# Performance work log

Measured on AMD Instinct MI355X. Metric: run time of the kernel, lower is better.

Reference implementation:

```python
import jax, jax.numpy as jnp
import numpy as np

B, S, D = 4, 2048, 1024
H = 16
DH = D // H          # 64
DFF = 4096
EPS = 1e-5


def _layer_norm(x, gamma, beta):
    mu = jnp.mean(x, axis=-1, keepdims=True)
    var = jnp.mean(jnp.square(x - mu), axis=-1, keepdims=True)
    return (x - mu) * jax.lax.rsqrt(var + EPS) * gamma + beta


def setup_inputs() -> dict:
    key = jax.random.key(0)
    ks = jax.random.split(key, 8)
    s_in = 1.0 / np.sqrt(D)
    s_ff = 1.0 / np.sqrt(DFF)
    return {
        "x": jax.random.normal(ks[0], (B, S, D), dtype=jnp.float32),
        # per-head qkv weights stacked: [H, D, 3*DH] (nn.Linear, bias=False)
        "Wqkv": jax.random.normal(ks[1], (H, D, 3 * DH), dtype=jnp.float32) * s_in,
        "Wproj": jax.random.normal(ks[2], (D, D), dtype=jnp.float32) * s_in,
        "bproj": jnp.zeros((D,), dtype=jnp.float32),
        "ln1_g": jnp.ones((D,), dtype=jnp.float32),
        "ln1_b": jnp.zeros((D,), dtype=jnp.float32),
        "ln2_g": jnp.ones((D,), dtype=jnp.float32),
        "ln2_b": jnp.zeros((D,), dtype=jnp.float32),
        "W1": jax.random.normal(ks[3], (D, DFF), dtype=jnp.float32) * s_in,
        "b1": jnp.zeros((DFF,), dtype=jnp.float32),
        "W2": jax.random.normal(ks[4], (DFF, D), dtype=jnp.float32) * s_ff,
        "b2": jnp.zeros((D,), dtype=jnp.float32),
    }


def reference(x, Wqkv, Wproj, bproj, ln1_g, ln1_b, ln2_g, ln2_b, W1, b1, W2, b2):
    # fused multi-head QKV projection: [B,S,D] x [H,D,3*DH] -> [B,H,S,3*DH]
    qkv = jnp.einsum('bsd,hde->bhse', x, Wqkv)
    q, k, v = jnp.split(qkv, 3, axis=-1)          # each [B,H,S,DH]
    scale = 1.0 / jnp.sqrt(jnp.asarray(DH, dtype=x.dtype))
    scores = jnp.einsum('bhsd,bhtd->bhst', q, k) * scale   # [B,H,S,S]
    causal = jnp.tril(jnp.ones((S, S), dtype=bool))
    scores = jnp.where(causal, scores, jnp.finfo(x.dtype).min)
    attn = jax.nn.softmax(scores, axis=-1)
    heads = jnp.einsum('bhst,bhtd->bhsd', attn, v)          # [B,H,S,DH]
    att_out = heads.transpose(0, 2, 1, 3).reshape(B, S, D)  # concat heads
    att_out = att_out @ Wproj + bproj
    out = _layer_norm(x + att_out, ln1_g, ln1_b)            # dropout = identity (eval)
    mlp_out = (jax.nn.gelu(out @ W1 + b1, approximate=False)) @ W2 + b2
    out = _layer_norm(out + mlp_out, ln2_g, ln2_b)
    return out
```

## Files before the change

### kernel.cpp

```cpp
#include <hip/hip_runtime.h>
#include <math.h>

#define BB 4
#define SS 2048
#define DD 1024
#define HH 16
#define DHH 64
#define DFF 4096
static constexpr float LN_EPS = 1e-5f;

typedef __bf16 bf16x8 __attribute__((ext_vector_type(8)));
typedef float f32x4 __attribute__((ext_vector_type(4)));
typedef unsigned short u16x8 __attribute__((ext_vector_type(8)));

__device__ inline unsigned short f2bf(float f) {
    union { float f; unsigned int u; } v; v.f = f;
    unsigned int u = v.u + 0x7FFFu + ((v.u >> 16) & 1u);
    return (unsigned short)(u >> 16);
}

__device__ __forceinline__ float fexp2(float x) {
    return __builtin_amdgcn_exp2f(x);
}

__device__ __forceinline__ void gl_lds16(const unsigned short* g,
                                         unsigned short* l) {
    __builtin_amdgcn_global_load_lds(
        (const __attribute__((address_space(1))) unsigned int*)g,
        (__attribute__((address_space(3))) unsigned int*)l, 16, 0, 0);
}

#define GBAR()                               \
    do {                                     \
        asm volatile("" ::: "memory");       \
        __builtin_amdgcn_s_barrier();        \
        asm volatile("" ::: "memory");       \
    } while (0)
#define VMCNT(n) asm volatile("s_waitcnt vmcnt(" #n ")" ::: "memory")

__global__ __launch_bounds__(256) void transpose_bf16_kernel(
    const float* __restrict__ in, unsigned short* __restrict__ outT,
    int R, int C) {
    __shared__ float t[64][65];
    const int r0 = blockIdx.y * 64, c0 = blockIdx.x * 64;
    const int cl = threadIdx.x & 63, rl = threadIdx.x >> 6;
#pragma unroll
    for (int rr = 0; rr < 16; ++rr)
        t[rl + rr * 4][cl] = in[(size_t)(r0 + rl + rr * 4) * C + c0 + cl];
    __syncthreads();
#pragma unroll
    for (int rr = 0; rr < 16; ++rr)
        outT[(size_t)(c0 + rl + rr * 4) * R + r0 + cl] = f2bf(t[cl][rl + rr * 4]);
}

__global__ __launch_bounds__(256) void repack_wqkv_bf16_kernel(
    const float* __restrict__ Wqkv, unsigned short* __restrict__ Wq2T) {
    __shared__ float t[64][65];
    const int h = blockIdx.z;
    const int d0 = blockIdx.y * 64, e0 = blockIdx.x * 64;
    const int cl = threadIdx.x & 63, rl = threadIdx.x >> 6;
#pragma unroll
    for (int rr = 0; rr < 16; ++rr)
        t[rl + rr * 4][cl] =
            Wqkv[((size_t)h * DD + d0 + rl + rr * 4) * 192 + e0 + cl];
    __syncthreads();
#pragma unroll
    for (int rr = 0; rr < 16; ++rr)
        Wq2T[((size_t)h * 192 + e0 + rl + rr * 4) * DD + d0 + cl] =
            f2bf(t[cl][rl + rr * 4]);
}

__global__ __launch_bounds__(256) void f2bf_kernel(
    const float* __restrict__ in, unsigned short* __restrict__ out, int n) {
    int i = blockIdx.x * 256 + threadIdx.x;
    if (i < n) out[i] = f2bf(in[i]);
}

template <int RS>
__device__ __forceinline__ void stage_half(const unsigned short* __restrict__ G,
                                           int ldK, int growbase, int kbase,
                                           unsigned short* lbase, int tid) {
#pragma unroll
    for (int s = 0; s < 2; ++s) {
        const int c16 = s * 512 + tid;
        const int r = c16 >> 3, c = c16 & 7;
        const int grow =
            growbase + ((r >> RS) << (RS + 1)) + (r & ((1 << RS) - 1));
        const int gcol = kbase + ((c ^ (r & 7)) << 3);
        gl_lds16(&G[(size_t)grow * ldK + gcol], &lbase[c16 << 3]);
    }
}

__device__ __forceinline__ void stage_64(const unsigned short* __restrict__ G,
                                         int ldK, int growbase, int kbase,
                                         unsigned short* lbase, int tid) {
    const int r = tid >> 3, c = tid & 7;
    const int grow = growbase + ((r >> 5) << 6) + (r & 31);
    const int gcol = kbase + ((c ^ (r & 7)) << 3);
    gl_lds16(&G[(size_t)grow * ldK + gcol], &lbase[tid << 3]);
}

__device__ __forceinline__ void read_afrag(const unsigned short* s, int base,
                                           int wm, int l15, int g,
                                           bf16x8 af[4][2]) {
#pragma unroll
    for (int ii = 0; ii < 4; ++ii) {
        const int lr = wm * 64 + ii * 16 + l15;
#pragma unroll
        for (int ks = 0; ks < 2; ++ks) {
            const int p = ((ks << 2) + g) ^ (lr & 7);
            af[ii][ks] = __builtin_bit_cast(
                bf16x8, *(const u16x8*)&s[base + lr * 64 + p * 8]);
        }
    }
}

__device__ __forceinline__ void read_bfrag(const unsigned short* s, int base,
                                           int wn, int l15, int g,
                                           bf16x8 bf2[2][2]) {
#pragma unroll
    for (int jj = 0; jj < 2; ++jj) {
        const int lr = wn * 32 + jj * 16 + l15;
#pragma unroll
        for (int ks = 0; ks < 2; ++ks) {
            const int p = ((ks << 2) + g) ^ (lr & 7);
            bf2[jj][ks] = __builtin_bit_cast(
                bf16x8, *(const u16x8*)&s[base + lr * 64 + p * 8]);
        }
    }
}

template <int MH, int NH>
__device__ __forceinline__ void mfma_quad(f32x4 acc[8][4],
                                          const bf16x8 af[4][2],
                                          const bf16x8 bf2[2][2]) {
    __builtin_amdgcn_s_setprio(1);
#pragma unroll
    for (int ks = 0; ks < 2; ++ks)
#pragma unroll
        for (int ii = 0; ii < 4; ++ii)
#pragma unroll
            for (int jj = 0; jj < 2; ++jj)
                acc[MH * 4 + ii][NH * 2 + jj] =
                    __builtin_amdgcn_mfma_f32_16x16x32_bf16(
                        af[ii][ks], bf2[jj][ks],
                        acc[MH * 4 + ii][NH * 2 + jj], 0, 0, 0);
    __builtin_amdgcn_s_setprio(0);
}

template <int MODE>
__global__ __launch_bounds__(512) void mfma_gemm256_kernel(
    const unsigned short* __restrict__ A, const unsigned short* __restrict__ BT,
    float* __restrict__ Cf, unsigned short* __restrict__ Cb,
    const float* __restrict__ bias, const float* __restrict__ resid,
    int M, int N, int K) {
    __shared__ __align__(16) unsigned short smem[65536];
    const int tid = threadIdx.x;
    const int lane = tid & 63, wave = tid >> 6;
    const int wm = wave >> 2, wn = wave & 3;
    const int l15 = lane & 15, g = lane >> 4;

    const int gx = gridDim.x, nwg = gx * gridDim.y;
    const int lid = blockIdx.y * gx + blockIdx.x;
    const int swz = ((nwg & 7) == 0) ? ((lid & 7) * (nwg >> 3) + (lid >> 3))
                                     : lid;
    const int row0 = (swz / gx) * 256;
    const int col0 = (swz % gx) * 256;

    const int kt = K >> 6;

    f32x4 acc[8][4] = {};

    stage_half<6>(A, K, row0, 0, smem + 0, tid);
    stage_half<6>(A, K, row0 + 64, 0, smem + 8192, tid);
    stage_half<5>(BT, K, col0, 0, smem + 32768, tid);
    stage_half<5>(BT, K, col0 + 32, 0, smem + 40960, tid);
    VMCNT(4);
    stage_half<6>(A, K, row0, 64, smem + 16384, tid);
    stage_half<6>(A, K, row0 + 64, 64, smem + 24576, tid);
    stage_half<5>(BT, K, col0, 64, smem + 49152, tid);
    VMCNT(6);
    GBAR();

    bf16x8 af[4][2], bf0[2][2], bf1[2][2];
    for (int it = 0; it < (kt >> 1); ++it) {
        const int t1k = (2 * it + 1) << 6;
        int t2 = 2 * it + 2; if (t2 > kt - 1) t2 = kt - 1;
        int t3 = 2 * it + 3; if (t3 > kt - 1) t3 = kt - 1;
        const int t2k = t2 << 6, t3k = t3 << 6;

        read_afrag(smem, 0, wm, l15, g, af);
        read_bfrag(smem, 32768, wn, l15, g, bf0);
        stage_half<5>(BT, K, col0 + 32, t1k, smem + 57344, tid);
        GBAR();
        mfma_quad<0, 0>(acc, af, bf0);
        GBAR();

        read_bfrag(smem, 40960, wn, l15, g, bf1);
        stage_half<6>(A, K, row0, t2k, smem + 0, tid);
        GBAR();
        mfma_quad<0, 1>(acc, af, bf1);
        GBAR();

        read_afrag(smem, 8192, wm, l15, g, af);
        stage_half<5>(BT, K, col0, t2k, smem + 32768, tid);
        GBAR();
        mfma_quad<1, 1>(acc, af, bf1);
        GBAR();

        stage_half<6>(A, K, row0 + 64, t2k, smem + 8192, tid);
        GBAR();
        mfma_quad<1, 0>(acc, af, bf0);
        VMCNT(6);
        GBAR();

        read_afrag(smem, 16384, wm, l15, g, af);
        read_bfrag(smem, 49152, wn, l15, g, bf0);
        stage_half<5>(BT, K, col0 + 32, t2k, smem + 40960, tid);
        GBAR();
        mfma_quad<0, 0>(acc, af, bf0);
        GBAR();

        read_bfrag(smem, 57344, wn, l15, g, bf1);
        stage_half<6>(A, K, row0, t3k, smem + 16384, tid);
        GBAR();
        mfma_quad<0, 1>(acc, af, bf1);
        GBAR();

        read_afrag(smem, 24576, wm, l15, g, af);
        stage_half<5>(BT, K, col0, t3k, smem + 49152, tid);
        GBAR();
        mfma_quad<1, 1>(acc, af, bf1);
        GBAR();

        stage_half<6>(A, K, row0 + 64, t3k, smem + 24576, tid);
        GBAR();
        mfma_quad<1, 0>(acc, af, bf0);
        VMCNT(6);
        GBAR();
    }
    VMCNT(0);
    GBAR();

    if (MODE == 2) {
        constexpr int SLAB = 264;
#pragma unroll
        for (int i2 = 0; i2 < 8; ++i2) {
            __syncthreads();
#pragma unroll
            for (int j2 = 0; j2 < 4; ++j2) {
                const int col = wn * 64 + j2 * 16 + l15;
                const float bv = bias[col0 + col];
#pragma unroll
                for (int r = 0; r < 4; ++r) {
                    float v = acc[i2][j2][r] + bv;
                    float t = fexp2(v * (2.30211849f + 0.10294198f * v * v));
                    float gel = v * t * __builtin_amdgcn_rcpf(t + 1.f);
                    smem[(wm * 16 + g * 4 + r) * SLAB + col] = f2bf(gel);
                }
            }
            __syncthreads();
            const int sr = tid >> 4;
            const int cc = (tid & 15) * 16;
            const int grow = row0 + ((sr >> 4) << 7) + i2 * 16 + (sr & 15);
            *(u16x8*)&Cb[(size_t)grow * N + col0 + cc] =
                *(const u16x8*)&smem[sr * SLAB + cc];
            *(u16x8*)&Cb[(size_t)grow * N + col0 + cc + 8] =
                *(const u16x8*)&smem[sr * SLAB + cc + 8];
        }
        return;
    }

#pragma unroll
    for (int i2 = 0; i2 < 8; ++i2) {
#pragma unroll
        for (int j2 = 0; j2 < 4; ++j2) {
            const int col = col0 + wn * 64 + j2 * 16 + l15;
            const int rowb = row0 + wm * 128 + i2 * 16 + g * 4;
            const float bv = bias[col];
#pragma unroll
            for (int r = 0; r < 4; ++r) {
                const int row = rowb + r;
                float v = acc[i2][j2][r] + bv + resid[(size_t)row * N + col];
                Cf[(size_t)row * N + col] = v;
            }
        }
    }
}

__device__ __forceinline__ void read_af128(const unsigned short* s, int base,
                                           int wm, int l15, int g,
                                           bf16x8 af[2][2]) {
#pragma unroll
    for (int ii = 0; ii < 2; ++ii) {
        const int lr = wm * 32 + ii * 16 + l15;
#pragma unroll
        for (int ks = 0; ks < 2; ++ks) {
            const int p = ((ks << 2) + g) ^ (lr & 7);
            af[ii][ks] = __builtin_bit_cast(
                bf16x8, *(const u16x8*)&s[base + lr * 64 + p * 8]);
        }
    }
}

__device__ __forceinline__ void read_bf128(const unsigned short* s, int base,
                                           int wn, int l15, int g,
                                           bf16x8 bf2[2][2]) {
#pragma unroll
    for (int jj = 0; jj < 2; ++jj) {
        const int lr = wn * 32 + jj * 16 + l15;
#pragma unroll
        for (int ks = 0; ks < 2; ++ks) {
            const int p = ((ks << 2) + g) ^ (lr & 7);
            bf2[jj][ks] = __builtin_bit_cast(
                bf16x8, *(const u16x8*)&s[base + lr * 64 + p * 8]);
        }
    }
}

template <int MH, int NH>
__device__ __forceinline__ void mfma_quad128(f32x4 acc[4][4],
                                             const bf16x8 af[2][2],
                                             const bf16x8 bf2[2][2]) {
    __builtin_amdgcn_s_setprio(1);
#pragma unroll
    for (int ks = 0; ks < 2; ++ks)
#pragma unroll
        for (int ii = 0; ii < 2; ++ii)
#pragma unroll
            for (int jj = 0; jj < 2; ++jj)
                acc[MH * 2 + ii][NH * 2 + jj] =
                    __builtin_amdgcn_mfma_f32_16x16x32_bf16(
                        af[ii][ks], bf2[jj][ks],
                        acc[MH * 2 + ii][NH * 2 + jj], 0, 0, 0);
    __builtin_amdgcn_s_setprio(0);
}

template <int MODE>
__global__ __launch_bounds__(512) void gemm_n128_kernel(
    const unsigned short* __restrict__ A, const unsigned short* __restrict__ BT,
    float* __restrict__ Cf, const float* __restrict__ bias,
    const float* __restrict__ resid, unsigned short* __restrict__ Qb,
    unsigned short* __restrict__ Kb, unsigned short* __restrict__ VTb,
    int M, int N, int K) {
    __shared__ __align__(16) unsigned short smem[49152];
    const int tid = threadIdx.x;
    const int lane = tid & 63, wave = tid >> 6;
    const int wm = wave >> 1, wn = wave & 1;
    const int l15 = lane & 15, g = lane >> 4;

    const int gx = gridDim.x, nwg = gx * gridDim.y;
    const int lid = blockIdx.y * gx + blockIdx.x;
    const int swz = ((nwg & 7) == 0) ? ((lid & 7) * (nwg >> 3) + (lid >> 3))
                                     : lid;
    const int row0 = (swz / gx) * 256;
    const int col0 = (swz % gx) * 128;

    const int kt = K >> 6;

    f32x4 acc[4][4] = {};

    stage_half<5>(A, K, row0, 0, smem + 0, tid);
    stage_half<5>(A, K, row0 + 32, 0, smem + 8192, tid);
    stage_64(BT, K, col0, 0, smem + 32768, tid);
    stage_64(BT, K, col0 + 32, 0, smem + 36864, tid);
    VMCNT(4);
    stage_half<5>(A, K, row0, 64, smem + 16384, tid);
    stage_half<5>(A, K, row0 + 32, 64, smem + 24576, tid);
    stage_64(BT, K, col0, 64, smem + 40960, tid);
    VMCNT(5);
    GBAR();

    bf16x8 af[2][2], bf0[2][2], bf1[2][2];
    for (int it = 0; it < (kt >> 1); ++it) {
        const int t1k = (2 * it + 1) << 6;
        int t2 = 2 * it + 2; if (t2 > kt - 1) t2 = kt - 1;
        int t3 = 2 * it + 3; if (t3 > kt - 1) t3 = kt - 1;
        const int t2k = t2 << 6, t3k = t3 << 6;

        read_af128(smem, 0, wm, l15, g, af);
        read_bf128(smem, 32768, wn, l15, g, bf0);
        stage_64(BT, K, col0 + 32, t1k, smem + 45056, tid);
        GBAR();
        mfma_quad128<0, 0>(acc, af, bf0);
        GBAR();

        read_bf128(smem, 36864, wn, l15, g, bf1);
        stage_half<5>(A, K, row0, t2k, smem + 0, tid);
        GBAR();
        mfma_quad128<0, 1>(acc, af, bf1);
        GBAR();

        read_af128(smem, 8192, wm, l15, g, af);
        stage_64(BT, K, col0, t2k, smem + 32768, tid);
        GBAR();
        mfma_quad128<1, 1>(acc, af, bf1);
        GBAR();

        stage_half<5>(A, K, row0 + 32, t2k, smem + 8192, tid);
        GBAR();
        mfma_quad128<1, 0>(acc, af, bf0);
        VMCNT(5);
        GBAR();

        read_af128(smem, 16384, wm, l15, g, af);
        read_bf128(smem, 40960, wn, l15, g, bf0);
        stage_64(BT, K, col0 + 32, t2k, smem + 36864, tid);
        GBAR();
        mfma_quad128<0, 0>(acc, af, bf0);
        GBAR();

        read_bf128(smem, 45056, wn, l15, g, bf1);
        stage_half<5>(A, K, row0, t3k, smem + 16384, tid);
        GBAR();
        mfma_quad128<0, 1>(acc, af, bf1);
        GBAR();

        read_af128(smem, 24576, wm, l15, g, af);
        stage_64(BT, K, col0, t3k, smem + 40960, tid);
        GBAR();
        mfma_quad128<1, 1>(acc, af, bf1);
        GBAR();

        stage_half<5>(A, K, row0 + 32, t3k, smem + 24576, tid);
        GBAR();
        mfma_quad128<1, 0>(acc, af, bf0);
        VMCNT(5);
        GBAR();
    }
    VMCNT(0);
    GBAR();

#pragma unroll
    for (int i2 = 0; i2 < 4; ++i2) {
#pragma unroll
        for (int j2 = 0; j2 < 4; ++j2) {
            const int col = col0 + wn * 64 + j2 * 16 + l15;
            const int rowb = row0 + wm * 64 + i2 * 16 + g * 4;
            if (MODE == 4) {
                const int h = col / 192, e = col % 192;
                const int bb = rowb >> 11, s = rowb & 2047;
                if (e < 64) {
                    unsigned short* q =
                        Qb + (((size_t)bb * HH + h) * SS + s) * 64 + e;
#pragma unroll
                    for (int r = 0; r < 4; ++r)
                        q[r * 64] = f2bf(acc[i2][j2][r] * 0.18033688f);
                } else if (e < 128) {
                    unsigned short* kp =
                        Kb + (((size_t)bb * HH + h) * SS + s) * 64 + (e - 64);
#pragma unroll
                    for (int r = 0; r < 4; ++r)
                        kp[r * 64] = f2bf(acc[i2][j2][r]);
                } else {
                    ushort4 pk;
                    pk.x = f2bf(acc[i2][j2][0]);
                    pk.y = f2bf(acc[i2][j2][1]);
                    pk.z = f2bf(acc[i2][j2][2]);
                    pk.w = f2bf(acc[i2][j2][3]);
                    *(ushort4*)(VTb + (((size_t)bb * HH + h) * 64 + (e - 128)) *
                                          SS + s) = pk;
                }
            } else {
                const float bv = bias[col];
#pragma unroll
                for (int r = 0; r < 4; ++r) {
                    const int row = rowb + r;
                    float v = acc[i2][j2][r] + bv + resid[(size_t)row * N + col];
                    Cf[(size_t)row * N + col] = v;
                }
            }
        }
    }
}

__global__ __launch_bounds__(256) void fattn_kernel(
    const unsigned short* __restrict__ Qb, const unsigned short* __restrict__ Kb,
    const unsigned short* __restrict__ VTb, unsigned short* __restrict__ att) {
    constexpr int QSTR = 68, KSTR = 68, VSTR = 76, PSTR = 68;
    __shared__ __align__(16) unsigned short Pls[128 * PSTR];
    __shared__ __align__(16) unsigned short Kls[64 * KSTR];
    __shared__ __align__(16) unsigned short VTls[64 * VSTR];

    const int bh = blockIdx.x;
    const int q0 = blockIdx.y * 128;
    const int tid = threadIdx.x;
    const int lane = tid & 63;
    const int wave = tid >> 6;
    const int l15 = lane & 15;
    const int g = lane >> 4;
    const int b = bh >> 4, h = bh & 15;

    const unsigned short* Qh = Qb + (size_t)bh * SS * 64;
    const unsigned short* Kh = Kb + (size_t)bh * SS * 64;
    const unsigned short* Vh = VTb + (size_t)bh * 64 * SS;

    {
        const int row = tid >> 1, c0 = (tid & 1) * 32;
        const unsigned short* src = Qh + (size_t)(q0 + row) * 64 + c0;
        unsigned short* dst = &Pls[row * QSTR + c0];
#pragma unroll
        for (int c = 0; c < 32; c += 8)
            *(u16x8*)(dst + c) = *(const u16x8*)(src + c);
    }
    __syncthreads();
    bf16x8 qf[2][2];
#pragma unroll
    for (int i = 0; i < 2; ++i)
#pragma unroll
        for (int ks = 0; ks < 2; ++ks)
            qf[i][ks] = __builtin_bit_cast(
                bf16x8, *(const u16x8*)&Pls[(wave * 32 + i * 16 + l15) * QSTR +
                                            ks * 32 + g * 8]);
    __syncthreads();

    f32x4 oacc[4][2] = {};
    float mst[2], lst[2];
#pragma unroll
    for (int i = 0; i < 2; ++i) { mst[i] = -1e30f; lst[i] = 0.f; }

    const int srow = tid >> 2, sc0 = (tid & 3) * 16;
    const int qlim = q0 + wave * 32 + 31;
    const int qrow = wave * 32 + l15;

    for (int t0 = 0; t0 <= q0 + 64; t0 += 64) {
        __syncthreads();
        {
            const unsigned short* ksrc = Kh + (size_t)(t0 + srow) * 64 + sc0;
            *(u16x8*)&Kls[srow * KSTR + sc0]     = *(const u16x8*)ksrc;
            *(u16x8*)&Kls[srow * KSTR + sc0 + 8] = *(const u16x8*)(ksrc + 8);
            const unsigned short* vsrc = Vh + (size_t)srow * SS + t0 + sc0;
            *(u16x8*)&VTls[srow * VSTR + sc0]     = *(const u16x8*)vsrc;
            *(u16x8*)&VTls[srow * VSTR + sc0 + 8] = *(const u16x8*)(vsrc + 8);
        }
        __syncthreads();
        if (t0 > qlim) continue;

        f32x4 sacc[4][2] = {};
#pragma unroll
        for (int ks = 0; ks < 2; ++ks) {
            bf16x8 kb[4];
#pragma unroll
            for (int j = 0; j < 4; ++j)
                kb[j] = __builtin_bit_cast(
                    bf16x8, *(const u16x8*)&Kls[(j * 16 + l15) * KSTR +
                                                ks * 32 + g * 8]);
#pragma unroll
            for (int j = 0; j < 4; ++j)
#pragma unroll
                for (int i = 0; i < 2; ++i)
                    sacc[j][i] = __builtin_amdgcn_mfma_f32_16x16x32_bf16(
                        kb[j], qf[i][ks], sacc[j][i], 0, 0, 0);
        }

        if (t0 >= q0) {
#pragma unroll
            for (int j = 0; j < 4; ++j)
#pragma unroll
                for (int i = 0; i < 2; ++i)
#pragma unroll
                    for (int r = 0; r < 4; ++r) {
                        const int kg = t0 + j * 16 + g * 4 + r;
                        const int qg = q0 + qrow + i * 16;
                        if (kg > qg) sacc[j][i][r] = -1e30f;
                    }
        }

#pragma unroll
        for (int i = 0; i < 2; ++i) {
            float mx = -1e30f;
#pragma unroll
            for (int j = 0; j < 4; ++j)
#pragma unroll
                for (int r = 0; r < 4; ++r) mx = fmaxf(mx, sacc[j][i][r]);
            mx = fmaxf(mx, __shfl_xor(mx, 16));
            mx = fmaxf(mx, __shfl_xor(mx, 32));
            const float mn = fmaxf(mst[i], mx);
            const float al = fexp2(mst[i] - mn);
            mst[i] = mn;
            float rsum = 0.f;
            const int pbase = (qrow + i * 16) * PSTR + g * 4;
#pragma unroll
            for (int j = 0; j < 4; ++j) {
                float p0 = fexp2(sacc[j][i][0] - mn);
                float p1 = fexp2(sacc[j][i][1] - mn);
                float p2 = fexp2(sacc[j][i][2] - mn);
                float p3 = fexp2(sacc[j][i][3] - mn);
                rsum += (p0 + p1) + (p2 + p3);
                ushort4 pk;
                pk.x = f2bf(p0); pk.y = f2bf(p1);
                pk.z = f2bf(p2); pk.w = f2bf(p3);
                *(ushort4*)&Pls[pbase + j * 16] = pk;
            }
            rsum += __shfl_xor(rsum, 16);
            rsum += __shfl_xor(rsum, 32);
            lst[i] = lst[i] * al + rsum;
#pragma unroll
            for (int jo = 0; jo < 4; ++jo)
#pragma unroll
                for (int r = 0; r < 4; ++r) oacc[jo][i][r] *= al;
        }
        __syncthreads();

#pragma unroll
        for (int ks = 0; ks < 2; ++ks) {
            bf16x8 vb[4], pf[2];
#pragma unroll
            for (int jo = 0; jo < 4; ++jo)
                vb[jo] = __builtin_bit_cast(
                    bf16x8, *(const u16x8*)&VTls[(jo * 16 + l15) * VSTR +
                                                 ks * 32 + g * 8]);
#pragma unroll
            for (int i = 0; i < 2; ++i)
                pf[i] = __builtin_bit_cast(
                    bf16x8, *(const u16x8*)&Pls[(qrow + i * 16) * PSTR +
                                                ks * 32 + g * 8]);
#pragma unroll
            for (int jo = 0; jo < 4; ++jo)
#pragma unroll
                for (int i = 0; i < 2; ++i)
                    oacc[jo][i] = __builtin_amdgcn_mfma_f32_16x16x32_bf16(
                        vb[jo], pf[i], oacc[jo][i], 0, 0, 0);
        }
    }

#pragma unroll
    for (int i = 0; i < 2; ++i) {
        const float inv = 1.f / lst[i];
        const int qg = q0 + qrow + i * 16;
        unsigned short* dst = att + ((size_t)b * SS + qg) * DD + h * 64 + g * 4;
#pragma unroll
        for (int jo = 0; jo < 4; ++jo) {
            ushort4 pk;
            pk.x = f2bf(oacc[jo][i][0] * inv);
            pk.y = f2bf(oacc[jo][i][1] * inv);
            pk.z = f2bf(oacc[jo][i][2] * inv);
            pk.w = f2bf(oacc[jo][i][3] * inv);
            *(ushort4*)(dst + jo * 16) = pk;
        }
    }
}

__global__ __launch_bounds__(256) void ln_kernel(
    const float* __restrict__ X, const float* __restrict__ g,
    const float* __restrict__ bta, float* __restrict__ Y,
    unsigned short* __restrict__ Yb) {
    const int row = blockIdx.x;
    const float4 xv = ((const float4*)(X + (size_t)row * DD))[threadIdx.x];

    __shared__ float red1[4], red2[4];
    float s = xv.x + xv.y + xv.z + xv.w;
#pragma unroll
    for (int off = 32; off > 0; off >>= 1) s += __shfl_down(s, off);
    const int wave = threadIdx.x >> 6;
    if ((threadIdx.x & 63) == 0) red1[wave] = s;
    __syncthreads();
    const float mu = (red1[0] + red1[1] + red1[2] + red1[3]) * (1.f / DD);

    float dx = xv.x - mu, dy = xv.y - mu, dz = xv.z - mu, dw = xv.w - mu;
    float s2 = dx * dx + dy * dy + dz * dz + dw * dw;
#pragma unroll
    for (int off = 32; off > 0; off >>= 1) s2 += __shfl_down(s2, off);
    if ((threadIdx.x & 63) == 0) red2[wave] = s2;
    __syncthreads();
    const float var = (red2[0] + red2[1] + red2[2] + red2[3]) * (1.f / DD);
    const float rstd = rsqrtf(var + LN_EPS);

    const float4 gv = ((const float4*)g)[threadIdx.x];
    const float4 bv = ((const float4*)bta)[threadIdx.x];
    float4 yv;
    yv.x = dx * rstd * gv.x + bv.x;
    yv.y = dy * rstd * gv.y + bv.y;
    yv.z = dz * rstd * gv.z + bv.z;
    yv.w = dw * rstd * gv.w + bv.w;
    ((float4*)(Y + (size_t)row * DD))[threadIdx.x] = yv;
    if (Yb) {
        ushort4 q;
        q.x = f2bf(yv.x); q.y = f2bf(yv.y);
        q.z = f2bf(yv.z); q.w = f2bf(yv.w);
        ((ushort4*)(Yb + (size_t)row * DD))[threadIdx.x] = q;
    }
}

extern "C" void kernel_launch(void* const* d_in, const int* in_sizes, int n_in,
                              void* d_out, int out_size, void* d_ws,
                              size_t ws_size, hipStream_t stream) {
    const float* x     = (const float*)d_in[0];
    const float* Wqkv  = (const float*)d_in[1];
    const float* Wproj = (const float*)d_in[2];
    const float* bproj = (const float*)d_in[3];
    const float* ln1_g = (const float*)d_in[4];
    const float* ln1_b = (const float*)d_in[5];
    const float* ln2_g = (const float*)d_in[6];
    const float* ln2_b = (const float*)d_in[7];
    const float* W1    = (const float*)d_in[8];
    const float* b1    = (const float*)d_in[9];
    const float* W2    = (const float*)d_in[10];
    const float* b2    = (const float*)d_in[11];
    float* out = (float*)d_out;

    const size_t M = (size_t)BB * SS;
    const size_t MB = 1024 * 1024;
    char* w = (char*)d_ws;
    unsigned short* Qb     = (unsigned short*)(w + 0);
    unsigned short* out1b  = (unsigned short*)(w + 0);
    unsigned short* Kb     = (unsigned short*)(w + 16 * MB);
    unsigned short* VTb    = (unsigned short*)(w + 32 * MB);
    unsigned short* hbuf   = (unsigned short*)(w + 16 * MB);
    unsigned short* Wq2T   = (unsigned short*)(w + 96 * MB);
    unsigned short* xb     = (unsigned short*)(w + 102 * MB);
    unsigned short* att    = (unsigned short*)(w + 96 * MB);
    float*          out1   = (float*)(w + 96 * MB);
    unsigned short* WprojT = (unsigned short*)(w + 118 * MB);
    unsigned short* W1T    = (unsigned short*)(w + 128 * MB);
    unsigned short* W2T    = (unsigned short*)(w + 136 * MB);

    repack_wqkv_bf16_kernel<<<dim3(3, 16, 16), 256, 0, stream>>>(Wqkv, Wq2T);
    transpose_bf16_kernel<<<dim3(16, 16), 256, 0, stream>>>(Wproj, WprojT, 1024, 1024);
    transpose_bf16_kernel<<<dim3(64, 16), 256, 0, stream>>>(W1, W1T, 1024, 4096);
    transpose_bf16_kernel<<<dim3(16, 64), 256, 0, stream>>>(W2, W2T, 4096, 1024);
    f2bf_kernel<<<(int)((M * DD + 255) / 256), 256, 0, stream>>>(x, xb, (int)(M * DD));

    gemm_n128_kernel<4><<<dim3(3072 / 128, M / 256), 512, 0, stream>>>(
        xb, Wq2T, nullptr, nullptr, nullptr, Qb, Kb, VTb, (int)M, 3072, 1024);

    fattn_kernel<<<dim3(BB * HH, SS / 128), 256, 0, stream>>>(Qb, Kb, VTb, att);

    gemm_n128_kernel<3><<<dim3(1024 / 128, M / 256), 512, 0, stream>>>(
        att, WprojT, out, bproj, x, nullptr, nullptr, nullptr,
        (int)M, 1024, 1024);

    ln_kernel<<<(int)M, 256, 0, stream>>>(out, ln1_g, ln1_b, out1, out1b);

    mfma_gemm256_kernel<2><<<dim3(4096 / 256, M / 256), 512, 0, stream>>>(
        out1b, W1T, nullptr, hbuf, b1, nullptr, (int)M, 4096, 1024);

    gemm_n128_kernel<3><<<dim3(1024 / 128, M / 256), 512, 0, stream>>>(
        hbuf, W2T, out, b2, out1, nullptr, nullptr, nullptr,
        (int)M, 1024, 4096);

    ln_kernel<<<(int)M, 256, 0, stream>>>(out, ln2_g, ln2_b, out, nullptr);
}
```

Before: 510.3 us.

## Double-buffer K/V tiles in flash attention with async global-to-LDS loads

Replaces the synchronous K/V register-staged copies with double-buffered, XOR-swizzled LDS tiles filled by global_load_lds, so the next tile's loads overlap the current tile's compute. It also drops syncthreads around Q staging, skips the rescale of the output accumulator when the running max does not grow, and switches f2bf to the native bf16 conversion. It adds LDS use and relies on each wave writing and reading only its own P and Q rows, which creates some risk around removed barriers.

```diff
diff --git a/kernel.cpp b/kernel.cpp
--- a/kernel.cpp
+++ b/kernel.cpp
@@ -13,10 +13,8 @@
 typedef float f32x4 __attribute__((ext_vector_type(4)));
 typedef unsigned short u16x8 __attribute__((ext_vector_type(8)));
 
-__device__ inline unsigned short f2bf(float f) {
-    union { float f; unsigned int u; } v; v.f = f;
-    unsigned int u = v.u + 0x7FFFu + ((v.u >> 16) & 1u);
-    return (unsigned short)(u >> 16);
+__device__ __forceinline__ unsigned short f2bf(float f) {
+    return __builtin_bit_cast(unsigned short, (__bf16)f);
 }
 
 __device__ __forceinline__ float fexp2(float x) {
@@ -98,6 +96,18 @@
     const int grow = growbase + ((r >> 5) << 6) + (r & 31);
     const int gcol = kbase + ((c ^ (r & 7)) << 3);
     gl_lds16(&G[(size_t)grow * ldK + gcol], &lbase[tid << 3]);
+}
+
+__device__ __forceinline__ void stage_kv(const unsigned short* __restrict__ src,
+                                         size_t rstride, unsigned short* dst,
+                                         int tid) {
+#pragma unroll
+    for (int s = 0; s < 2; ++s) {
+        const int c16 = s * 256 + tid;
+        const int r = c16 >> 3, c = c16 & 7;
+        gl_lds16(&src[(size_t)r * rstride + ((c ^ (r & 7)) << 3)],
+                 &dst[c16 << 3]);
+    }
 }
 
 __device__ __forceinline__ void read_afrag(const unsigned short* s, int base,
@@ -477,10 +487,10 @@
 __global__ __launch_bounds__(256) void fattn_kernel(
     const unsigned short* __restrict__ Qb, const unsigned short* __restrict__ Kb,
     const unsigned short* __restrict__ VTb, unsigned short* __restrict__ att) {
-    constexpr int QSTR = 68, KSTR = 68, VSTR = 76, PSTR = 68;
+    constexpr int PSTR = 68;
     __shared__ __align__(16) unsigned short Pls[128 * PSTR];
-    __shared__ __align__(16) unsigned short Kls[64 * KSTR];
-    __shared__ __align__(16) unsigned short VTls[64 * VSTR];
+    __shared__ __align__(16) unsigned short Kls[2][64 * 64];
+    __shared__ __align__(16) unsigned short VTls[2][64 * 64];
 
     const int bh = blockIdx.x;
     const int q0 = blockIdx.y * 128;
@@ -498,131 +508,144 @@
     {
         const int row = tid >> 1, c0 = (tid & 1) * 32;
         const unsigned short* src = Qh + (size_t)(q0 + row) * 64 + c0;
-        unsigned short* dst = &Pls[row * QSTR + c0];
+        unsigned short* dst = &Pls[row * PSTR + c0];
 #pragma unroll
         for (int c = 0; c < 32; c += 8)
             *(u16x8*)(dst + c) = *(const u16x8*)(src + c);
     }
-    __syncthreads();
     bf16x8 qf[2][2];
 #pragma unroll
     for (int i = 0; i < 2; ++i)
 #pragma unroll
         for (int ks = 0; ks < 2; ++ks)
             qf[i][ks] = __builtin_bit_cast(
-                bf16x8, *(const u16x8*)&Pls[(wave * 32 + i * 16 + l15) * QSTR +
+                bf16x8, *(const u16x8*)&Pls[(wave * 32 + i * 16 + l15) * PSTR +
                                             ks * 32 + g * 8]);
-    __syncthreads();
 
     f32x4 oacc[4][2] = {};
     float mst[2], lst[2];
 #pragma unroll
     for (int i = 0; i < 2; ++i) { mst[i] = -1e30f; lst[i] = 0.f; }
 
-    const int srow = tid >> 2, sc0 = (tid & 3) * 16;
     const int qlim = q0 + wave * 32 + 31;
     const int qrow = wave * 32 + l15;
-
-    for (int t0 = 0; t0 <= q0 + 64; t0 += 64) {
-        __syncthreads();
-        {
-            const unsigned short* ksrc = Kh + (size_t)(t0 + srow) * 64 + sc0;
-            *(u16x8*)&Kls[srow * KSTR + sc0]     = *(const u16x8*)ksrc;
-            *(u16x8*)&Kls[srow * KSTR + sc0 + 8] = *(const u16x8*)(ksrc + 8);
-            const unsigned short* vsrc = Vh + (size_t)srow * SS + t0 + sc0;
-            *(u16x8*)&VTls[srow * VSTR + sc0]     = *(const u16x8*)vsrc;
-            *(u16x8*)&VTls[srow * VSTR + sc0 + 8] = *(const u16x8*)(vsrc + 8);
-        }
-        __syncthreads();
-        if (t0 > qlim) continue;
-
-        f32x4 sacc[4][2] = {};
-#pragma unroll
-        for (int ks = 0; ks < 2; ++ks) {
-            bf16x8 kb[4];
-#pragma unroll
-            for (int j = 0; j < 4; ++j)
-                kb[j] = __builtin_bit_cast(
-                    bf16x8, *(const u16x8*)&Kls[(j * 16 + l15) * KSTR +
-                                                ks * 32 + g * 8]);
-#pragma unroll
-            for (int j = 0; j < 4; ++j)
+    const int nt = (q0 >> 6) + 2;
+    const int xh = l15 & 7;
+
+    stage_kv(Kh, 64, &Kls[0][0], tid);
+    stage_kv(Vh, SS, &VTls[0][0], tid);
+
+    for (int t = 0; t < nt; ++t) {
+        const int t0 = t << 6;
+        const int tn = (t + 1 < nt) ? t + 1 : nt - 1;
+        stage_kv(Kh + (size_t)(tn << 6) * 64, 64, &Kls[(t + 1) & 1][0], tid);
+        stage_kv(Vh + (tn << 6), SS, &VTls[(t + 1) & 1][0], tid);
+        VMCNT(4);
+        GBAR();
+
+        if (t0 <= qlim) {
+            const unsigned short* Kt = &Kls[t & 1][0];
+            const unsigned short* Vt = &VTls[t & 1][0];
+
+            f32x4 sacc[4][2] = {};
+#pragma unroll
+            for (int ks = 0; ks < 2; ++ks) {
+                const int ko = ((((ks << 2) + g) ^ xh) << 3);
+                bf16x8 kb[4];
+#pragma unroll
+                for (int j = 0; j < 4; ++j)
+                    kb[j] = __builtin_bit_cast(
+                        bf16x8, *(const u16x8*)&Kt[(j * 16 + l15) * 64 + ko]);
+#pragma unroll
+                for (int j = 0; j < 4; ++j)
+#pragma unroll
+                    for (int i = 0; i < 2; ++i)
+                        sacc[j][i] = __builtin_amdgcn_mfma_f32_16x16x32_bf16(
+                            kb[j], qf[i][ks], sacc[j][i], 0, 0, 0);
+            }
+
+            if (t0 >= q0) {
+#pragma unroll
+                for (int j = 0; j < 4; ++j)
+#pragma unroll
+                    for (int i = 0; i < 2; ++i)
+#pragma unroll
+                        for (int r = 0; r < 4; ++r) {
+                            const int kg = t0 + j * 16 + g * 4 + r;
+                            const int qg = q0 + qrow + i * 16;
+                            if (kg > qg) sacc[j][i][r] = -1e30f;
+                        }
+            }
+
+#pragma unroll
+            for (int i = 0; i < 2; ++i) {
+                float mx = -1e30f;
+#pragma unroll
+                for (int j = 0; j < 4; ++j)
+                    mx = fmaxf(mx,
+                               fmaxf(fmaxf(sacc[j][i][0], sacc[j][i][1]),
+                                     fmaxf(sacc[j][i][2], sacc[j][i][3])));
+                mx = fmaxf(mx, __shfl_xor(mx, 16));
+                mx = fmaxf(mx, __shfl_xor(mx, 32));
+                const bool grow = !__all(mx <= mst[i]);
+                float al = 1.f;
+                if (grow) {
+                    const float mn = fmaxf(mst[i], mx);
+                    al = fexp2(mst[i] - mn);
+                    mst[i] = mn;
+                }
+                const float mm = mst[i];
+                float rsum = 0.f;
+                const int pbase = (qrow + i * 16) * PSTR + g * 4;
+#pragma unroll
+                for (int j = 0; j < 4; ++j) {
+                    float p0 = fexp2(sacc[j][i][0] - mm);
+                    float p1 = fexp2(sacc[j][i][1] - mm);
+                    float p2 = fexp2(sacc[j][i][2] - mm);
+                    float p3 = fexp2(sacc[j][i][3] - mm);
+                    rsum += (p0 + p1) + (p2 + p3);
+                    ushort4 pk;
+                    pk.x = f2bf(p0); pk.y = f2bf(p1);
+                    pk.z = f2bf(p2); pk.w = f2bf(p3);
+                    *(ushort4*)&Pls[pbase + j * 16] = pk;
+                }
+                rsum += __shfl_xor(rsum, 16);
+                rsum += __shfl_xor(rsum, 32);
+                if (grow) {
+                    lst[i] = lst[i] * al + rsum;
+#pragma unroll
+                    for (int jo = 0; jo < 4; ++jo)
+#pragma unroll
+                        for (int r = 0; r < 4; ++r) oacc[jo][i][r] *= al;
+                } else {
+                    lst[i] += rsum;
+                }
+            }
+
+#pragma unroll
+            for (int ks = 0; ks < 2; ++ks) {
+                const int ko = ((((ks << 2) + g) ^ xh) << 3);
+                bf16x8 vb[4], pf[2];
+#pragma unroll
+                for (int jo = 0; jo < 4; ++jo)
+                    vb[jo] = __builtin_bit_cast(
+                        bf16x8, *(const u16x8*)&Vt[(jo * 16 + l15) * 64 + ko]);
 #pragma unroll
                 for (int i = 0; i < 2; ++i)
-                    sacc[j][i] = __builtin_amdgcn_mfma_f32_16x16x32_bf16(
-                        kb[j], qf[i][ks], sacc[j][i], 0, 0, 0);
-        }
-
-        if (t0 >= q0) {
-#pragma unroll
-            for (int j = 0; j < 4; ++j)
-#pragma unroll
-                for (int i = 0; i < 2; ++i)
-#pragma unroll
-                    for (int r = 0; r < 4; ++r) {
-                        const int kg = t0 + j * 16 + g * 4 + r;
-                        const int qg = q0 + qrow + i * 16;
-                        if (kg > qg) sacc[j][i][r] = -1e30f;
-                    }
-        }
-
-#pragma unroll
-        for (int i = 0; i < 2; ++i) {
-            float mx = -1e30f;
-#pragma unroll
-            for (int j = 0; j < 4; ++j)
-#pragma unroll
-                for (int r = 0; r < 4; ++r) mx = fmaxf(mx, sacc[j][i][r]);
-            mx = fmaxf(mx, __shfl_xor(mx, 16));
-            mx = fmaxf(mx, __shfl_xor(mx, 32));
-            const float mn = fmaxf(mst[i], mx);
-            const float al = fexp2(mst[i] - mn);
-            mst[i] = mn;
-            float rsum = 0.f;
-            const int pbase = (qrow + i * 16) * PSTR + g * 4;
-#pragma unroll
-            for (int j = 0; j < 4; ++j) {
-                float p0 = fexp2(sacc[j][i][0] - mn);
-                float p1 = fexp2(sacc[j][i][1] - mn);
-                float p2 = fexp2(sacc[j][i][2] - mn);
-                float p3 = fexp2(sacc[j][i][3] - mn);
-                rsum += (p0 + p1) + (p2 + p3);
-                ushort4 pk;
-                pk.x = f2bf(p0); pk.y = f2bf(p1);
-                pk.z = f2bf(p2); pk.w = f2bf(p3);
-                *(ushort4*)&Pls[pbase + j * 16] = pk;
+                    pf[i] = __builtin_bit_cast(
+                        bf16x8, *(const u16x8*)&Pls[(qrow + i * 16) * PSTR +
+                                                    ks * 32 + g * 8]);
+#pragma unroll
+                for (int jo = 0; jo < 4; ++jo)
+#pragma unroll
+                    for (int i = 0; i < 2; ++i)
+                        oacc[jo][i] = __builtin_amdgcn_mfma_f32_16x16x32_bf16(
+                            vb[jo], pf[i], oacc[jo][i], 0, 0, 0);
             }
-            rsum += __shfl_xor(rsum, 16);
-            rsum += __shfl_xor(rsum, 32);
-            lst[i] = lst[i] * al + rsum;
-#pragma unroll
-            for (int jo = 0; jo < 4; ++jo)
-#pragma unroll
-                for (int r = 0; r < 4; ++r) oacc[jo][i][r] *= al;
-        }
-        __syncthreads();
-
-#pragma unroll
-        for (int ks = 0; ks < 2; ++ks) {
-            bf16x8 vb[4], pf[2];
-#pragma unroll
-            for (int jo = 0; jo < 4; ++jo)
-                vb[jo] = __builtin_bit_cast(
-                    bf16x8, *(const u16x8*)&VTls[(jo * 16 + l15) * VSTR +
-                                                 ks * 32 + g * 8]);
-#pragma unroll
-            for (int i = 0; i < 2; ++i)
-                pf[i] = __builtin_bit_cast(
-                    bf16x8, *(const u16x8*)&Pls[(qrow + i * 16) * PSTR +
-                                                ks * 32 + g * 8]);
-#pragma unroll
-            for (int jo = 0; jo < 4; ++jo)
-#pragma unroll
-                for (int i = 0; i < 2; ++i)
-                    oacc[jo][i] = __builtin_amdgcn_mfma_f32_16x16x32_bf16(
-                        vb[jo], pf[i], oacc[jo][i], 0, 0, 0);
-        }
-    }
+        }
+        GBAR();
+    }
+    VMCNT(0);
 
 #pragma unroll
     for (int i = 0; i < 2; ++i) {
```

New measurement: 505.3 us. Within noise of the previous version (-1.0%).
